# Performance work log

Measured on AMD Instinct MI355X. Metric: run time of the kernel, lower is better.

## Reference

```python
import jax, jax.numpy as jnp
import numpy as np

HEAD_SIZE = 64

def setup_inputs() -> dict:
    key = jax.random.key(0)
    k1, k2, k3, k4 = jax.random.split(key, 4)
    B, T, C = 4, 4096, 768
    s = 1.0 / np.sqrt(C)
    return {
        "x": jax.random.normal(k1, (B, T, C), dtype=jnp.float32),
        "Wq": jax.random.normal(k2, (C, HEAD_SIZE), dtype=jnp.float32) * s,
        "Wk": jax.random.normal(k3, (C, HEAD_SIZE), dtype=jnp.float32) * s,
        "Wv": jax.random.normal(k4, (C, HEAD_SIZE), dtype=jnp.float32) * s,
    }

def reference(x, Wq, Wk, Wv):
    # x: [B,T,C]; Wq/Wk/Wv: [C,H]
    T = x.shape[1]
    q = jnp.einsum('btc,ch->bth', x, Wq)
    k = jnp.einsum('btc,ch->bth', x, Wk)
    v = jnp.einsum('btc,ch->bth', x, Wv)
    scale = HEAD_SIZE ** (-0.5)
    wei = jnp.einsum('bth,bsh->bts', q, k) * scale  # [B,T,T]
    causal = jnp.tril(jnp.ones((T, T), dtype=bool))
    wei = jnp.where(causal, wei, -jnp.inf)
    wei = jax.nn.softmax(wei, axis=-1)
    # dropout p=0.0 -> identity
    out = jnp.einsum('bts,bsh->bth', wei, v)  # [B,T,H]
    return out
```

## Files before the change

### kernel.cpp

```cpp
#include <hip/hip_runtime.h>
#include <hip/hip_bf16.h>
#include <stdint.h>

typedef unsigned short u16;
typedef __attribute__((ext_vector_type(8))) __bf16 bf16x8;
typedef __attribute__((ext_vector_type(4))) float f32x4;

#define LOG2E 1.44269504088896340736f
#define FIXED_M 16.0f

__device__ inline u16 f2bf(float f){
  uint32_t u = __float_as_uint(f);
  u += 0x7FFFu + ((u >> 16) & 1u);
  return (u16)(u >> 16);
}
__device__ inline float bf2f(u16 v){
  return __uint_as_float(((uint32_t)v) << 16);
}

__global__ __launch_bounds__(256) void wt_kernel(const float* __restrict__ Wq,
                                                 const float* __restrict__ Wk,
                                                 const float* __restrict__ Wv,
                                                 u16* __restrict__ wtf){
  int idx = blockIdx.x * 256 + threadIdx.x;
  if (idx >= 192 * 768) return;
  int n = idx / 768, c = idx - n * 768;
  int h = n & 63;
  const float* W = (n < 64) ? Wq : ((n < 128) ? Wk : Wv);
  float v = W[c * 64 + h];
  if (n < 64) v *= 0.125f * LOG2E;
  int f = n >> 4, n16 = n & 15;
  int kstep = c >> 5, quad = (c >> 3) & 3, j = c & 7;
  wtf[(size_t)((f * 24 + kstep) * 64 + quad * 16 + n16) * 8 + j] = f2bf(v);
}

__global__ __launch_bounds__(256) void proj_kernel(const float* __restrict__ x,
                                                   const u16* __restrict__ wtf,
                                                   u16* __restrict__ qs,
                                                   u16* __restrict__ kso,
                                                   u16* __restrict__ vt){
  __shared__ u16 At[2 * 24 * 64 * 8];
  const int tid = threadIdx.x;
  const int w = tid >> 6, lane = tid & 63;
  const int n16 = lane & 15, quad = lane >> 4;
  const int rt = blockIdx.x * 32;

  const float* xb = x + (size_t)rt * 768;
  for (int p = 0; p < 3; ++p){
    float4 t[8];
#pragma unroll
    for (int i = 0; i < 8; ++i)
      t[i] = *(const float4*)(xb + (size_t)((p * 8 + i) * 256 + tid) * 4);
#pragma unroll
    for (int i = 0; i < 8; ++i){
      int l = (p * 8 + i) * 256 + tid;
      int row = l / 192, c4 = l - row * 192;
      int g = row >> 4, r16 = row & 15;
      int ksn = c4 >> 3, qd = (c4 >> 1) & 3, j0 = (c4 & 1) * 4;
      int idx = (((g * 24 + ksn) * 64 + qd * 16 + r16) * 8 + j0) ^ ((ksn & 7) << 3);
      union { ushort4 s; u16 e[4]; } pk;
      pk.e[0] = f2bf(t[i].x); pk.e[1] = f2bf(t[i].y);
      pk.e[2] = f2bf(t[i].z); pk.e[3] = f2bf(t[i].w);
      *(ushort4*)&At[idx] = pk.s;
    }
  }
  __syncthreads();

  const f32x4 fz = {0.f, 0.f, 0.f, 0.f};
  f32x4 acc[2][3];
#pragma unroll
  for (int g = 0; g < 2; ++g)
#pragma unroll
    for (int j = 0; j < 3; ++j) acc[g][j] = fz;

#pragma unroll
  for (int kst = 0; kst < 24; ++kst){
    const int sw = (kst & 7) << 3;
    bf16x8 a0 = *(const bf16x8*)&At[(((0 * 24 + kst) * 64 + lane) * 8) ^ sw];
    bf16x8 a1 = *(const bf16x8*)&At[(((1 * 24 + kst) * 64 + lane) * 8) ^ sw];
#pragma unroll
    for (int j = 0; j < 3; ++j){
      bf16x8 bfr = *(const bf16x8*)(wtf + (size_t)(((3 * w + j) * 24 + kst) * 64 + lane) * 8);
      acc[0][j] = __builtin_amdgcn_mfma_f32_16x16x32_bf16(a0, bfr, acc[0][j], 0, 0, 0);
      acc[1][j] = __builtin_amdgcn_mfma_f32_16x16x32_bf16(a1, bfr, acc[1][j], 0, 0, 0);
    }
  }

  const int bb = rt >> 12, t0 = rt & 4095;
#pragma unroll
  for (int j = 0; j < 3; ++j){
    const int F = 3 * w + j;
#pragma unroll
    for (int g = 0; g < 2; ++g){
#pragma unroll
      for (int r = 0; r < 4; ++r){
        u16 val = f2bf(acc[g][j][r]);
        int row = rt + g * 16 + quad * 4 + r;
        if (F < 4)
          qs[(size_t)row * 64 + F * 16 + n16] = val;
        else if (F < 8)
          kso[(size_t)row * 64 + (F - 4) * 16 + n16] = val;
        else
          vt[((size_t)bb * 64 + (F - 8) * 16 + n16) * 4096 + t0 + g * 16 + quad * 4 + r] = val;
      }
    }
  }
}

__global__ __launch_bounds__(256) void flash_part(const u16* __restrict__ qs,
                                                  const u16* __restrict__ ks,
                                                  const u16* __restrict__ vtg,
                                                  u16* __restrict__ Opart,
                                                  float* __restrict__ ml){
  const int b  = blockIdx.x >> 9;
  const int qt = (blockIdx.x >> 3) & 63;
  const int ck = blockIdx.x & 7;
  const int kt0 = ck * 8;
  if (kt0 > qt) return;
  const int kt1 = min(qt, kt0 + 7);

  __shared__ u16 Ks[64 * 72];
  __shared__ u16 Vt[64 * 72];
  __shared__ u16 Ps[4 * 16 * 72];
  const int tid = threadIdx.x;
  const int w = tid >> 6, lane = tid & 63;
  const int n16 = lane & 15, quad = lane >> 4;
  const size_t bo = (size_t)b * 4096 * 64;
  const u16* qb = qs + bo;
  const u16* kb = ks + bo;
  const u16* vb = vtg + bo;

  const int qrow = qt * 64 + w * 16 + n16;
  bf16x8 qA0 = *(const bf16x8*)(qb + (size_t)qrow * 64 + quad * 8);
  bf16x8 qA1 = *(const bf16x8*)(qb + (size_t)qrow * 64 + 32 + quad * 8);

  const f32x4 fz = {0.f, 0.f, 0.f, 0.f};
  f32x4 O[4];
  float rs[4] = {0.f, 0.f, 0.f, 0.f};
#pragma unroll
  for (int f = 0; f < 4; ++f) O[f] = fz;

  const int c0r = tid >> 3,          c0p = tid & 7;
  const int c1r = (tid + 256) >> 3,  c1p = tid & 7;

  uint4 rk0 = *(const uint4*)(kb + (size_t)kt0 * 4096 + c0r * 64 + c0p * 8);
  uint4 rk1 = *(const uint4*)(kb + (size_t)kt0 * 4096 + c1r * 64 + c1p * 8);
  uint4 rv0 = *(const uint4*)(vb + (size_t)c0r * 4096 + kt0 * 64 + c0p * 8);
  uint4 rv1 = *(const uint4*)(vb + (size_t)c1r * 4096 + kt0 * 64 + c1p * 8);

  for (int kt = kt0; kt <= kt1; ++kt){
    *(uint4*)&Ks[c0r * 72 + c0p * 8] = rk0;
    *(uint4*)&Ks[c1r * 72 + c1p * 8] = rk1;
    *(uint4*)&Vt[c0r * 72 + c0p * 8] = rv0;
    *(uint4*)&Vt[c1r * 72 + c1p * 8] = rv1;
    __syncthreads();

    if (kt < kt1){
      rk0 = *(const uint4*)(kb + (size_t)(kt + 1) * 4096 + c0r * 64 + c0p * 8);
      rk1 = *(const uint4*)(kb + (size_t)(kt + 1) * 4096 + c1r * 64 + c1p * 8);
      rv0 = *(const uint4*)(vb + (size_t)c0r * 4096 + (kt + 1) * 64 + c0p * 8);
      rv1 = *(const uint4*)(vb + (size_t)c1r * 4096 + (kt + 1) * 64 + c1p * 8);
    }

    f32x4 S[4];
#pragma unroll
    for (int f = 0; f < 4; ++f){
      bf16x8 b0 = *(const bf16x8*)&Ks[(f * 16 + n16) * 72 + quad * 8];
      bf16x8 b1 = *(const bf16x8*)&Ks[(f * 16 + n16) * 72 + 32 + quad * 8];
      f32x4 s = fz;
      s = __builtin_amdgcn_mfma_f32_16x16x32_bf16(qA0, b0, s, 0, 0, 0);
      s = __builtin_amdgcn_mfma_f32_16x16x32_bf16(qA1, b1, s, 0, 0, 0);
      S[f] = s;
    }

    if (kt == qt){
#pragma unroll
      for (int f = 0; f < 4; ++f){
#pragma unroll
        for (int r = 0; r < 4; ++r){
          int col = kt * 64 + f * 16 + n16;
          int row = qt * 64 + w * 16 + quad * 4 + r;
          if (col > row) S[f][r] = -1e30f;
        }
      }
    }

#pragma unroll
    for (int f = 0; f < 4; ++f){
#pragma unroll
      for (int r = 0; r < 4; ++r){
        float p = __builtin_amdgcn_exp2f(S[f][r] - FIXED_M);
        S[f][r] = p;
        rs[r] += p;
      }
    }

#pragma unroll
    for (int f = 0; f < 4; ++f){
#pragma unroll
      for (int r = 0; r < 4; ++r)
        Ps[(w * 16 + quad * 4 + r) * 72 + f * 16 + n16] = f2bf(S[f][r]);
    }
    bf16x8 pA0 = *(const bf16x8*)&Ps[(w * 16 + n16) * 72 + quad * 8];
    bf16x8 pA1 = *(const bf16x8*)&Ps[(w * 16 + n16) * 72 + 32 + quad * 8];

#pragma unroll
    for (int f = 0; f < 4; ++f){
      bf16x8 v0 = *(const bf16x8*)&Vt[(f * 16 + n16) * 72 + quad * 8];
      bf16x8 v1 = *(const bf16x8*)&Vt[(f * 16 + n16) * 72 + 32 + quad * 8];
      O[f] = __builtin_amdgcn_mfma_f32_16x16x32_bf16(pA0, v0, O[f], 0, 0, 0);
      O[f] = __builtin_amdgcn_mfma_f32_16x16x32_bf16(pA1, v1, O[f], 0, 0, 0);
    }
    __syncthreads();
  }

#pragma unroll
  for (int r = 0; r < 4; ++r){
#pragma unroll
    for (int off = 1; off < 16; off <<= 1)
      rs[r] += __shfl_xor(rs[r], off, 16);
  }

  const size_t oidx = (size_t)blockIdx.x * 4096;
#pragma unroll
  for (int f = 0; f < 4; ++f){
#pragma unroll
    for (int r = 0; r < 4; ++r){
      int row_local = w * 16 + quad * 4 + r;
      Opart[oidx + (size_t)row_local * 64 + f * 16 + n16] = f2bf(O[f][r]);
    }
  }
  if (n16 == 0){
    float* lp = ml + (size_t)blockIdx.x * 64;
#pragma unroll
    for (int r = 0; r < 4; ++r)
      lp[w * 16 + quad * 4 + r] = rs[r];
  }
}

__global__ __launch_bounds__(256) void combine_kernel(const u16* __restrict__ Opart,
                                                      const float* __restrict__ ml,
                                                      float* __restrict__ out){
  const int gid = blockIdx.x * 256 + threadIdx.x;
  const size_t base = (size_t)gid * 4;
  const int bq = gid >> 10;
  const int rem = (int)(base & 4095);
  const int row = rem >> 6;
  const int qt = bq & 63;
  const int nc = (qt >> 3) + 1;

  float L = 0.f;
  float a0 = 0.f, a1 = 0.f, a2 = 0.f, a3 = 0.f;
  for (int c = 0; c < nc; ++c){
    L += ml[((size_t)bq * 8 + c) * 64 + row];
    const u16* p = Opart + ((size_t)bq * 8 + c) * 4096 + rem;
    uint2 d = *(const uint2*)p;
    a0 += bf2f((u16)(d.x & 0xffffu));
    a1 += bf2f((u16)(d.x >> 16));
    a2 += bf2f((u16)(d.y & 0xffffu));
    a3 += bf2f((u16)(d.y >> 16));
  }
  const float invL = 1.0f / L;
  float4 v = {a0 * invL, a1 * invL, a2 * invL, a3 * invL};
  *(float4*)(out + base) = v;
}

extern "C" void kernel_launch(void* const* d_in, const int* in_sizes, int n_in,
                              void* d_out, int out_size, void* d_ws, size_t ws_size,
                              hipStream_t stream){
  const float* x  = (const float*)d_in[0];
  const float* Wq = (const float*)d_in[1];
  const float* Wk = (const float*)d_in[2];
  const float* Wv = (const float*)d_in[3];
  float* out = (float*)d_out;

  u16* qs = (u16*)d_ws;
  u16* ks = qs + (size_t)16384 * 64;
  u16* vt = ks + (size_t)16384 * 64;
  u16* wtf = vt + (size_t)16384 * 64;
  u16* Opart = wtf + (size_t)192 * 768;
  float* ml = (float*)(Opart + (size_t)2048 * 4096);

  wt_kernel<<<576, 256, 0, stream>>>(Wq, Wk, Wv, wtf);
  proj_kernel<<<512, 256, 0, stream>>>(x, wtf, qs, ks, vt);
  flash_part<<<2048, 256, 0, stream>>>(qs, ks, vt, Opart, ml);
  combine_kernel<<<1024, 256, 0, stream>>>(Opart, ml, out);
}
```

Measured before the change: 141.2 us.

## Pre-swizzle K and V into MFMA fragment layout, load directly to registers

The projection kernel now stages its outputs through shared memory and writes K and V in a fragment-ordered layout that matches the MFMA B-operand per lane. The flash kernel then loads K and V fragments straight from global memory into registers, with K prefetched one tile ahead. This removes the shared-memory staging of K and V and both per-iteration __syncthreads in the attention loop. In exchange, all four waves now fetch the same K/V data redundantly from global or L2, which raises register pressure and cache traffic.

```diff
diff --git a/kernel.cpp b/kernel.cpp
--- a/kernel.cpp
+++ b/kernel.cpp
@@ -37,8 +37,8 @@
 __global__ __launch_bounds__(256) void proj_kernel(const float* __restrict__ x,
                                                    const u16* __restrict__ wtf,
                                                    u16* __restrict__ qs,
-                                                   u16* __restrict__ kso,
-                                                   u16* __restrict__ vt){
+                                                   u16* __restrict__ ksf,
+                                                   u16* __restrict__ vtf){
   __shared__ u16 At[2 * 24 * 64 * 8];
   const int tid = threadIdx.x;
   const int w = tid >> 6, lane = tid & 63;
@@ -85,31 +85,51 @@
       acc[1][j] = __builtin_amdgcn_mfma_f32_16x16x32_bf16(a1, bfr, acc[1][j], 0, 0, 0);
     }
   }
-
-  const int bb = rt >> 12, t0 = rt & 4095;
+  __syncthreads();
+
 #pragma unroll
   for (int j = 0; j < 3; ++j){
     const int F = 3 * w + j;
+    const int s = F >> 2, c0 = (F & 3) * 16;
 #pragma unroll
     for (int g = 0; g < 2; ++g){
 #pragma unroll
       for (int r = 0; r < 4; ++r){
         u16 val = f2bf(acc[g][j][r]);
-        int row = rt + g * 16 + quad * 4 + r;
-        if (F < 4)
-          qs[(size_t)row * 64 + F * 16 + n16] = val;
-        else if (F < 8)
-          kso[(size_t)row * 64 + (F - 4) * 16 + n16] = val;
-        else
-          vt[((size_t)bb * 64 + (F - 8) * 16 + n16) * 4096 + t0 + g * 16 + quad * 4 + r] = val;
+        int row = g * 16 + quad * 4 + r;
+        if (s < 2) At[s * 2304 + row * 72 + c0 + n16] = val;
+        else       At[4608 + (c0 + n16) * 40 + row]   = val;
       }
     }
   }
+  __syncthreads();
+
+  const int bb = rt >> 12, t0 = rt & 4095;
+  const int kt = t0 >> 6, f0 = (rt >> 4) & 3, half0 = (rt >> 5) & 1;
+  {
+    int row = tid >> 3, hc = tid & 7;
+    uint4 qv = *(const uint4*)&At[row * 72 + hc * 8];
+    *(uint4*)(qs + (size_t)(rt + row) * 64 + hc * 8) = qv;
+  }
+  {
+    int fi = tid >> 7, half = (tid >> 6) & 1, l2 = tid & 63;
+    int nn = l2 & 15, qq = l2 >> 4;
+    uint4 kv = *(const uint4*)&At[2304 + (fi * 16 + nn) * 72 + half * 32 + qq * 8];
+    size_t off = ((((size_t)(bb * 64 + kt) * 4 + f0 + fi) * 2 + half) * 64 + l2) * 8;
+    *(uint4*)(ksf + off) = kv;
+  }
+  {
+    int f = tid >> 6, l2 = tid & 63;
+    int nn = l2 & 15, qq = l2 >> 4;
+    uint4 vv = *(const uint4*)&At[4608 + (f * 16 + nn) * 40 + qq * 8];
+    size_t off = ((((size_t)(bb * 64 + kt) * 4 + f) * 2 + half0) * 64 + l2) * 8;
+    *(uint4*)(vtf + off) = vv;
+  }
 }
 
 __global__ __launch_bounds__(256) void flash_part(const u16* __restrict__ qs,
-                                                  const u16* __restrict__ ks,
-                                                  const u16* __restrict__ vtg,
+                                                  const u16* __restrict__ ksf,
+                                                  const u16* __restrict__ vtf,
                                                   u16* __restrict__ Opart,
                                                   float* __restrict__ ml){
   const int b  = blockIdx.x >> 9;
@@ -119,16 +139,14 @@
   if (kt0 > qt) return;
   const int kt1 = min(qt, kt0 + 7);
 
-  __shared__ u16 Ks[64 * 72];
-  __shared__ u16 Vt[64 * 72];
   __shared__ u16 Ps[4 * 16 * 72];
   const int tid = threadIdx.x;
   const int w = tid >> 6, lane = tid & 63;
   const int n16 = lane & 15, quad = lane >> 4;
-  const size_t bo = (size_t)b * 4096 * 64;
-  const u16* qb = qs + bo;
-  const u16* kb = ks + bo;
-  const u16* vb = vtg + bo;
+
+  const u16* qb = qs + (size_t)b * 262144;
+  const u16* kp = ksf + (size_t)b * 262144 + (size_t)kt0 * 4096 + lane * 8;
+  const u16* vp = vtf + (size_t)b * 262144 + (size_t)kt0 * 4096 + lane * 8;
 
   const int qrow = qt * 64 + w * 16 + n16;
   bf16x8 qA0 = *(const bf16x8*)(qb + (size_t)qrow * 64 + quad * 8);
@@ -140,37 +158,29 @@
 #pragma unroll
   for (int f = 0; f < 4; ++f) O[f] = fz;
 
-  const int c0r = tid >> 3,          c0p = tid & 7;
-  const int c1r = (tid + 256) >> 3,  c1p = tid & 7;
-
-  uint4 rk0 = *(const uint4*)(kb + (size_t)kt0 * 4096 + c0r * 64 + c0p * 8);
-  uint4 rk1 = *(const uint4*)(kb + (size_t)kt0 * 4096 + c1r * 64 + c1p * 8);
-  uint4 rv0 = *(const uint4*)(vb + (size_t)c0r * 4096 + kt0 * 64 + c0p * 8);
-  uint4 rv1 = *(const uint4*)(vb + (size_t)c1r * 4096 + kt0 * 64 + c1p * 8);
+  bf16x8 kf[8];
+#pragma unroll
+  for (int i = 0; i < 8; ++i) kf[i] = *(const bf16x8*)(kp + i * 512);
 
   for (int kt = kt0; kt <= kt1; ++kt){
-    *(uint4*)&Ks[c0r * 72 + c0p * 8] = rk0;
-    *(uint4*)&Ks[c1r * 72 + c1p * 8] = rk1;
-    *(uint4*)&Vt[c0r * 72 + c0p * 8] = rv0;
-    *(uint4*)&Vt[c1r * 72 + c1p * 8] = rv1;
-    __syncthreads();
+    bf16x8 vf[8];
+#pragma unroll
+    for (int i = 0; i < 8; ++i)
+      vf[i] = *(const bf16x8*)(vp + (size_t)(kt - kt0) * 4096 + i * 512);
+
+    f32x4 S[4];
+#pragma unroll
+    for (int f = 0; f < 4; ++f){
+      f32x4 s = fz;
+      s = __builtin_amdgcn_mfma_f32_16x16x32_bf16(qA0, kf[f * 2],     s, 0, 0, 0);
+      s = __builtin_amdgcn_mfma_f32_16x16x32_bf16(qA1, kf[f * 2 + 1], s, 0, 0, 0);
+      S[f] = s;
+    }
 
     if (kt < kt1){
-      rk0 = *(const uint4*)(kb + (size_t)(kt + 1) * 4096 + c0r * 64 + c0p * 8);
-      rk1 = *(const uint4*)(kb + (size_t)(kt + 1) * 4096 + c1r * 64 + c1p * 8);
-      rv0 = *(const uint4*)(vb + (size_t)c0r * 4096 + (kt + 1) * 64 + c0p * 8);
-      rv1 = *(const uint4*)(vb + (size_t)c1r * 4096 + (kt + 1) * 64 + c1p * 8);
-    }
-
-    f32x4 S[4];
-#pragma unroll
-    for (int f = 0; f < 4; ++f){
-      bf16x8 b0 = *(const bf16x8*)&Ks[(f * 16 + n16) * 72 + quad * 8];
-      bf16x8 b1 = *(const bf16x8*)&Ks[(f * 16 + n16) * 72 + 32 + quad * 8];
-      f32x4 s = fz;
-      s = __builtin_amdgcn_mfma_f32_16x16x32_bf16(qA0, b0, s, 0, 0, 0);
-      s = __builtin_amdgcn_mfma_f32_16x16x32_bf16(qA1, b1, s, 0, 0, 0);
-      S[f] = s;
+#pragma unroll
+      for (int i = 0; i < 8; ++i)
+        kf[i] = *(const bf16x8*)(kp + (size_t)(kt - kt0 + 1) * 4096 + i * 512);
     }
 
     if (kt == qt){
@@ -206,12 +216,9 @@
 
 #pragma unroll
     for (int f = 0; f < 4; ++f){
-      bf16x8 v0 = *(const bf16x8*)&Vt[(f * 16 + n16) * 72 + quad * 8];
-      bf16x8 v1 = *(const bf16x8*)&Vt[(f * 16 + n16) * 72 + 32 + quad * 8];
-      O[f] = __builtin_amdgcn_mfma_f32_16x16x32_bf16(pA0, v0, O[f], 0, 0, 0);
-      O[f] = __builtin_amdgcn_mfma_f32_16x16x32_bf16(pA1, v1, O[f], 0, 0, 0);
-    }
-    __syncthreads();
+      O[f] = __builtin_amdgcn_mfma_f32_16x16x32_bf16(pA0, vf[f * 2],     O[f], 0, 0, 0);
+      O[f] = __builtin_amdgcn_mfma_f32_16x16x32_bf16(pA1, vf[f * 2 + 1], O[f], 0, 0, 0);
+    }
   }
 
 #pragma unroll
@@ -274,15 +281,15 @@
   const float* Wv = (const float*)d_in[3];
   float* out = (float*)d_out;
 
-  u16* qs = (u16*)d_ws;
-  u16* ks = qs + (size_t)16384 * 64;
-  u16* vt = ks + (size_t)16384 * 64;
-  u16* wtf = vt + (size_t)16384 * 64;
+  u16* qs  = (u16*)d_ws;
+  u16* ksf = qs  + (size_t)16384 * 64;
+  u16* vtf = ksf + (size_t)16384 * 64;
+  u16* wtf = vtf + (size_t)16384 * 64;
   u16* Opart = wtf + (size_t)192 * 768;
   float* ml = (float*)(Opart + (size_t)2048 * 4096);
 
   wt_kernel<<<576, 256, 0, stream>>>(Wq, Wk, Wv, wtf);
-  proj_kernel<<<512, 256, 0, stream>>>(x, wtf, qs, ks, vt);
-  flash_part<<<2048, 256, 0, stream>>>(qs, ks, vt, Opart, ml);
+  proj_kernel<<<512, 256, 0, stream>>>(x, wtf, qs, ksf, vtf);
+  flash_part<<<2048, 256, 0, stream>>>(qs, ksf, vtf, Opart, ml);
   combine_kernel<<<1024, 256, 0, stream>>>(Opart, ml, out);
 }
```

Result: no change. 142.6 us (+1.0%).
